# Kernel optimization log

Measured on AMD Instinct MI355X. Metric: run time of the kernel, lower is better.

## Reference

```python
import jax, jax.numpy as jnp
import numpy as np

B, N_INST, H, W = 8, 64, 480, 480
EPS = 1e-12  # torch F.normalize eps


def setup_inputs() -> dict:
    key = jax.random.key(0)
    k1, k2, k3, k4, k5, k6 = jax.random.split(key, 6)
    # binary instance masks (output of connected-component labeling in the original)
    instance_masks = (jax.random.uniform(k1, (N_INST, H, W)) < 0.3).astype(jnp.float32)
    sample_ids = jax.random.randint(k2, (N_INST,), 0, B, dtype=jnp.int64)
    quaternion = jax.random.normal(k3, (B, 4, H, W), dtype=jnp.float32)
    scales = jax.random.normal(k4, (B, 3, H, W), dtype=jnp.float32)
    xy = jax.random.normal(k5, (B, 2, H, W), dtype=jnp.float32)
    z = jax.random.normal(k6, (B, H, W), dtype=jnp.float32)
    return {"instance_masks": instance_masks, "sample_ids": sample_ids,
            "quaternion": quaternion, "scales": scales, "xy": xy, "z": z}


def reference(instance_masks, sample_ids, quaternion, scales, xy, z):
    # instance_masks: [N,H,W] binary float; sample_ids: [N] in [0,B)
    mask_size = jnp.sum(instance_masks, axis=(-2, -1))  # [N]

    def masked_mean(d):  # d: [N,C,H,W] -> [N,C]
        return jnp.einsum('nhw,nchw->nc', instance_masks, d) / mask_size[:, None]

    # quaternion: masked mean then L2-normalize along channel dim
    q_agg = masked_mean(quaternion[sample_ids])                       # [N,4]
    q_agg = q_agg / jnp.maximum(jnp.linalg.norm(q_agg, axis=1, keepdims=True), EPS)
    # scales: masked mean
    s_agg = masked_mean(scales[sample_ids])                           # [N,3]
    # z: masked mean of [N,1,H,W] then exp
    z_agg = jnp.exp(masked_mean(z[sample_ids][:, None]))              # [N,1]
    # xy: masked dense map (passed on to hough voting downstream)
    xy_masked = instance_masks[:, None] * xy[sample_ids]              # [N,2,H,W]
    return q_agg, s_agg, z_agg, xy_masked
```

## Files before the change

### kernel.cpp

```cpp
#include <hip/hip_runtime.h>
#include <math.h>

#define HW      (480 * 480)
#define HW4     (HW / 4)
#define NINST   64
#define NB      8
#define NV      9
#define THREADS 256
#define NCHUNK  (HW4 / THREADS)

__global__ __launch_bounds__(THREADS) void agg_main(
    const float* __restrict__ masks,
    const int*   __restrict__ sids,
    const float* __restrict__ quat,
    const float* __restrict__ scales,
    const float* __restrict__ xy,
    const float* __restrict__ z,
    float*       __restrict__ out,
    float*       __restrict__ part)
{
    const int c   = blockIdx.x;
    const int b   = blockIdx.y;
    const int tid = threadIdx.x;
    const int i   = c * THREADS + tid;

    const float4* Q  = (const float4*)quat;
    const float4* S  = (const float4*)scales;
    const float4* X  = (const float4*)xy;
    const float4* Z  = (const float4*)z;
    const float4* M  = (const float4*)masks;
    float4*       O  = (float4*)(out + 512);

    const size_t qb = (size_t)b * 4 * HW4 + i;
    const float4 vq0 = Q[qb + 0 * HW4];
    const float4 vq1 = Q[qb + 1 * HW4];
    const float4 vq2 = Q[qb + 2 * HW4];
    const float4 vq3 = Q[qb + 3 * HW4];
    const size_t sb = (size_t)b * 3 * HW4 + i;
    const float4 vs0 = S[sb + 0 * HW4];
    const float4 vs1 = S[sb + 1 * HW4];
    const float4 vs2 = S[sb + 2 * HW4];
    const size_t xb = (size_t)b * 2 * HW4 + i;
    const float4 vx0 = X[xb + 0 * HW4];
    const float4 vx1 = X[xb + 1 * HW4];
    const float4 vz  = Z[(size_t)b * HW4 + i];

    __shared__ float sred[4][NV];
    const int lane = tid & 63;
    const int wid  = tid >> 6;

    for (int n = 0; n < NINST; ++n) {
        if (sids[n] != b) continue;

        const float4 m = M[(size_t)n * HW4 + i];

        O[((size_t)n * 2 + 0) * HW4 + i] =
            make_float4(m.x * vx0.x, m.y * vx0.y, m.z * vx0.z, m.w * vx0.w);
        O[((size_t)n * 2 + 1) * HW4 + i] =
            make_float4(m.x * vx1.x, m.y * vx1.y, m.z * vx1.z, m.w * vx1.w);

        float vals[NV];
        vals[0] = (m.x + m.y) + (m.z + m.w);
        vals[1] = m.x*vq0.x + m.y*vq0.y + m.z*vq0.z + m.w*vq0.w;
        vals[2] = m.x*vq1.x + m.y*vq1.y + m.z*vq1.z + m.w*vq1.w;
        vals[3] = m.x*vq2.x + m.y*vq2.y + m.z*vq2.z + m.w*vq2.w;
        vals[4] = m.x*vq3.x + m.y*vq3.y + m.z*vq3.z + m.w*vq3.w;
        vals[5] = m.x*vs0.x + m.y*vs0.y + m.z*vs0.z + m.w*vs0.w;
        vals[6] = m.x*vs1.x + m.y*vs1.y + m.z*vs1.z + m.w*vs1.w;
        vals[7] = m.x*vs2.x + m.y*vs2.y + m.z*vs2.z + m.w*vs2.w;
        vals[8] = m.x*vz.x  + m.y*vz.y  + m.z*vz.z  + m.w*vz.w;

#pragma unroll
        for (int v = 0; v < NV; ++v) {
            float x = vals[v];
#pragma unroll
            for (int off = 32; off > 0; off >>= 1)
                x += __shfl_down(x, off, 64);
            if (lane == 0) sred[wid][v] = x;
        }
        __syncthreads();
        if (tid < NV)
            part[((size_t)n * NCHUNK + c) * NV + tid] =
                (sred[0][tid] + sred[1][tid]) + (sred[2][tid] + sred[3][tid]);
        __syncthreads();
    }
}

__global__ __launch_bounds__(THREADS) void agg_final(
    const float* __restrict__ part,
    float*       __restrict__ out)
{
    const int n   = blockIdx.x;
    const int tid = threadIdx.x;

    float vals[NV];
#pragma unroll
    for (int v = 0; v < NV; ++v) vals[v] = 0.0f;
    for (int c = tid; c < NCHUNK; c += THREADS) {
        const float* p = part + ((size_t)n * NCHUNK + c) * NV;
#pragma unroll
        for (int v = 0; v < NV; ++v) vals[v] += p[v];
    }

    __shared__ float sred[4][NV];
    const int lane = tid & 63;
    const int wid  = tid >> 6;
#pragma unroll
    for (int v = 0; v < NV; ++v) {
        float x = vals[v];
#pragma unroll
        for (int off = 32; off > 0; off >>= 1)
            x += __shfl_down(x, off, 64);
        if (lane == 0) sred[wid][v] = x;
    }
    __syncthreads();

    if (tid == 0) {
        float s[NV];
#pragma unroll
        for (int v = 0; v < NV; ++v)
            s[v] = (sred[0][v] + sred[1][v]) + (sred[2][v] + sred[3][v]);

        const float inv = 1.0f / s[0];
        const float q0 = s[1] * inv, q1 = s[2] * inv, q2 = s[3] * inv, q3 = s[4] * inv;
        const float norm = sqrtf(q0*q0 + q1*q1 + q2*q2 + q3*q3);
        const float d = fmaxf(norm, 1e-12f);
        out[n * 4 + 0] = q0 / d;
        out[n * 4 + 1] = q1 / d;
        out[n * 4 + 2] = q2 / d;
        out[n * 4 + 3] = q3 / d;

        out[256 + n * 3 + 0] = s[5] * inv;
        out[256 + n * 3 + 1] = s[6] * inv;
        out[256 + n * 3 + 2] = s[7] * inv;

        out[448 + n] = expf(s[8] * inv);
    }
}

extern "C" void kernel_launch(void* const* d_in, const int* in_sizes, int n_in,
                              void* d_out, int out_size, void* d_ws, size_t ws_size,
                              hipStream_t stream) {
    const float* masks  = (const float*)d_in[0];
    const int*   sids   = (const int*)d_in[1];
    const float* quat   = (const float*)d_in[2];
    const float* scales = (const float*)d_in[3];
    const float* xy     = (const float*)d_in[4];
    const float* z      = (const float*)d_in[5];
    float* out  = (float*)d_out;
    float* part = (float*)d_ws;

    dim3 grid(NCHUNK, NB);
    agg_main<<<grid, THREADS, 0, stream>>>(masks, sids, quat, scales, xy, z, out, part);
    agg_final<<<NINST, THREADS, 0, stream>>>(part, out);
}
```

Measured before the change: 245.6 us.

## Group instances per block with grid-stride accumulation over pixels

Each block now builds a shared list of the instances that belong to its batch and walks them in groups of four. A grid-stride pixel loop accumulates register partial sums for all four instances at once. This cuts the per-instance block-wide shuffle reduction and __syncthreads pairs, and it raises memory-level parallelism by issuing several mask loads together. In exchange, batch feature data is reread once per group instead of held in registers, and register pressure goes up from the 36 accumulators. The partial-sum buffer shrinks to a fixed 128 blocks per instance.

```diff
diff --git a/kernel.cpp b/kernel.cpp
--- a/kernel.cpp
+++ b/kernel.cpp
@@ -6,8 +6,13 @@
 #define NINST   64
 #define NB      8
 #define NV      9
+#define GI      4
+#define NBLK    128
 #define THREADS 256
-#define NCHUNK  (HW4 / THREADS)
+
+__device__ __forceinline__ float dot4(const float4 a, const float4 b) {
+    return (a.x * b.x + a.y * b.y) + (a.z * b.z + a.w * b.w);
+}
 
 __global__ __launch_bounds__(THREADS) void agg_main(
     const float* __restrict__ masks,
@@ -19,69 +24,117 @@
     float*       __restrict__ out,
     float*       __restrict__ part)
 {
-    const int c   = blockIdx.x;
+    const int tid = threadIdx.x;
+    const int bx  = blockIdx.x;
     const int b   = blockIdx.y;
-    const int tid = threadIdx.x;
-    const int i   = c * THREADS + tid;
-
-    const float4* Q  = (const float4*)quat;
-    const float4* S  = (const float4*)scales;
-    const float4* X  = (const float4*)xy;
-    const float4* Z  = (const float4*)z;
+
+    __shared__ int   ilist[NINST];
+    __shared__ int   scnt;
+    __shared__ float sred[4][GI * NV];
+
+    if (tid == 0) {
+        int c = 0;
+        for (int n = 0; n < NINST; ++n)
+            if (sids[n] == b) ilist[c++] = n;
+        scnt = c;
+    }
+    __syncthreads();
+    const int cnt = scnt;
+
     const float4* M  = (const float4*)masks;
+    const float4* Q  = (const float4*)quat   + (size_t)b * 4 * HW4;
+    const float4* S  = (const float4*)scales + (size_t)b * 3 * HW4;
+    const float4* X  = (const float4*)xy     + (size_t)b * 2 * HW4;
+    const float4* Zp = (const float4*)z      + (size_t)b * HW4;
     float4*       O  = (float4*)(out + 512);
 
-    const size_t qb = (size_t)b * 4 * HW4 + i;
-    const float4 vq0 = Q[qb + 0 * HW4];
-    const float4 vq1 = Q[qb + 1 * HW4];
-    const float4 vq2 = Q[qb + 2 * HW4];
-    const float4 vq3 = Q[qb + 3 * HW4];
-    const size_t sb = (size_t)b * 3 * HW4 + i;
-    const float4 vs0 = S[sb + 0 * HW4];
-    const float4 vs1 = S[sb + 1 * HW4];
-    const float4 vs2 = S[sb + 2 * HW4];
-    const size_t xb = (size_t)b * 2 * HW4 + i;
-    const float4 vx0 = X[xb + 0 * HW4];
-    const float4 vx1 = X[xb + 1 * HW4];
-    const float4 vz  = Z[(size_t)b * HW4 + i];
-
-    __shared__ float sred[4][NV];
     const int lane = tid & 63;
     const int wid  = tid >> 6;
 
-    for (int n = 0; n < NINST; ++n) {
-        if (sids[n] != b) continue;
-
-        const float4 m = M[(size_t)n * HW4 + i];
-
-        O[((size_t)n * 2 + 0) * HW4 + i] =
-            make_float4(m.x * vx0.x, m.y * vx0.y, m.z * vx0.z, m.w * vx0.w);
-        O[((size_t)n * 2 + 1) * HW4 + i] =
-            make_float4(m.x * vx1.x, m.y * vx1.y, m.z * vx1.z, m.w * vx1.w);
-
-        float vals[NV];
-        vals[0] = (m.x + m.y) + (m.z + m.w);
-        vals[1] = m.x*vq0.x + m.y*vq0.y + m.z*vq0.z + m.w*vq0.w;
-        vals[2] = m.x*vq1.x + m.y*vq1.y + m.z*vq1.z + m.w*vq1.w;
-        vals[3] = m.x*vq2.x + m.y*vq2.y + m.z*vq2.z + m.w*vq2.w;
-        vals[4] = m.x*vq3.x + m.y*vq3.y + m.z*vq3.z + m.w*vq3.w;
-        vals[5] = m.x*vs0.x + m.y*vs0.y + m.z*vs0.z + m.w*vs0.w;
-        vals[6] = m.x*vs1.x + m.y*vs1.y + m.z*vs1.z + m.w*vs1.w;
-        vals[7] = m.x*vs2.x + m.y*vs2.y + m.z*vs2.z + m.w*vs2.w;
-        vals[8] = m.x*vz.x  + m.y*vz.y  + m.z*vz.z  + m.w*vz.w;
-
-#pragma unroll
-        for (int v = 0; v < NV; ++v) {
-            float x = vals[v];
-#pragma unroll
-            for (int off = 32; off > 0; off >>= 1)
-                x += __shfl_down(x, off, 64);
-            if (lane == 0) sred[wid][v] = x;
+    for (int g0 = 0; g0 < cnt; g0 += GI) {
+        int  nidx[GI];
+        bool valid[GI];
+#pragma unroll
+        for (int j = 0; j < GI; ++j) {
+            valid[j] = (g0 + j < cnt);
+            nidx[j]  = ilist[valid[j] ? (g0 + j) : (cnt - 1)];
         }
+
+        float acc[GI][NV];
+#pragma unroll
+        for (int j = 0; j < GI; ++j)
+#pragma unroll
+            for (int v = 0; v < NV; ++v) acc[j][v] = 0.0f;
+
+        for (int i = bx * THREADS + tid; i < HW4; i += NBLK * THREADS) {
+            float4 m[GI];
+#pragma unroll
+            for (int j = 0; j < GI; ++j)
+                m[j] = M[(size_t)nidx[j] * HW4 + i];
+
+            const float4 vx0 = X[i];
+            const float4 vx1 = X[HW4 + i];
+#pragma unroll
+            for (int j = 0; j < GI; ++j) {
+                if (valid[j]) {
+                    O[((size_t)nidx[j] * 2 + 0) * HW4 + i] = make_float4(
+                        m[j].x * vx0.x, m[j].y * vx0.y, m[j].z * vx0.z, m[j].w * vx0.w);
+                    O[((size_t)nidx[j] * 2 + 1) * HW4 + i] = make_float4(
+                        m[j].x * vx1.x, m[j].y * vx1.y, m[j].z * vx1.z, m[j].w * vx1.w);
+                }
+            }
+
+#pragma unroll
+            for (int j = 0; j < GI; ++j)
+                acc[j][0] += (m[j].x + m[j].y) + (m[j].z + m[j].w);
+
+            float4 t;
+            t = Q[0 * HW4 + i];
+#pragma unroll
+            for (int j = 0; j < GI; ++j) acc[j][1] += dot4(m[j], t);
+            t = Q[1 * HW4 + i];
+#pragma unroll
+            for (int j = 0; j < GI; ++j) acc[j][2] += dot4(m[j], t);
+            t = Q[2 * HW4 + i];
+#pragma unroll
+            for (int j = 0; j < GI; ++j) acc[j][3] += dot4(m[j], t);
+            t = Q[3 * HW4 + i];
+#pragma unroll
+            for (int j = 0; j < GI; ++j) acc[j][4] += dot4(m[j], t);
+            t = S[0 * HW4 + i];
+#pragma unroll
+            for (int j = 0; j < GI; ++j) acc[j][5] += dot4(m[j], t);
+            t = S[1 * HW4 + i];
+#pragma unroll
+            for (int j = 0; j < GI; ++j) acc[j][6] += dot4(m[j], t);
+            t = S[2 * HW4 + i];
+#pragma unroll
+            for (int j = 0; j < GI; ++j) acc[j][7] += dot4(m[j], t);
+            t = Zp[i];
+#pragma unroll
+            for (int j = 0; j < GI; ++j) acc[j][8] += dot4(m[j], t);
+        }
+
+#pragma unroll
+        for (int j = 0; j < GI; ++j)
+#pragma unroll
+            for (int v = 0; v < NV; ++v) {
+                float x = acc[j][v];
+#pragma unroll
+                for (int off = 32; off > 0; off >>= 1)
+                    x += __shfl_down(x, off, 64);
+                if (lane == 0) sred[wid][j * NV + v] = x;
+            }
         __syncthreads();
-        if (tid < NV)
-            part[((size_t)n * NCHUNK + c) * NV + tid] =
-                (sred[0][tid] + sred[1][tid]) + (sred[2][tid] + sred[3][tid]);
+        if (tid < GI * NV) {
+            const int j = tid / NV;
+            const int v = tid - j * NV;
+            if (g0 + j < cnt) {
+                const int n = ilist[g0 + j];
+                part[((size_t)n * NBLK + bx) * NV + v] =
+                    (sred[0][tid] + sred[1][tid]) + (sred[2][tid] + sred[3][tid]);
+            }
+        }
         __syncthreads();
     }
 }
@@ -96,8 +149,8 @@
     float vals[NV];
 #pragma unroll
     for (int v = 0; v < NV; ++v) vals[v] = 0.0f;
-    for (int c = tid; c < NCHUNK; c += THREADS) {
-        const float* p = part + ((size_t)n * NCHUNK + c) * NV;
+    for (int c = tid; c < NBLK; c += THREADS) {
+        const float* p = part + ((size_t)n * NBLK + c) * NV;
 #pragma unroll
         for (int v = 0; v < NV; ++v) vals[v] += p[v];
     }
@@ -123,7 +176,7 @@
 
         const float inv = 1.0f / s[0];
         const float q0 = s[1] * inv, q1 = s[2] * inv, q2 = s[3] * inv, q3 = s[4] * inv;
-        const float norm = sqrtf(q0*q0 + q1*q1 + q2*q2 + q3*q3);
+        const float norm = sqrtf(q0 * q0 + q1 * q1 + q2 * q2 + q3 * q3);
         const float d = fmaxf(norm, 1e-12f);
         out[n * 4 + 0] = q0 / d;
         out[n * 4 + 1] = q1 / d;
@@ -150,7 +203,7 @@
     float* out  = (float*)d_out;
     float* part = (float*)d_ws;
 
-    dim3 grid(NCHUNK, NB);
+    dim3 grid(NBLK, NB);
     agg_main<<<grid, THREADS, 0, stream>>>(masks, sids, quat, scales, xy, z, out, part);
     agg_final<<<NINST, THREADS, 0, stream>>>(part, out);
 }
```

Result: slower. 262.0 us (+6.7%).
